# Performance work log

Measured on AMD Instinct MI355X. Metric: run time of the kernel, lower is better.

The kernel has to match this reference:

```python
import jax, jax.numpy as jnp
import numpy as np

_LN2 = 0.6931471805599453
B, N, C, R, K = 256, 4096, 256, 32, 128
MAX_SPAN = 20.0
W_WEIGHT, W_COACT, W_SPAN = 1.0, 1.0, 0.3


def setup_inputs() -> dict:
    key = jax.random.key(0)
    k1, k2, k3, k4, k5 = jax.random.split(key, 5)
    A = jax.random.normal(k1, (B, N), dtype=jnp.float32)            # accumulated atom activations
    span_t = jax.random.uniform(k2, (B,), dtype=jnp.float32) * MAX_SPAN
    proto_weights = jax.random.normal(k3, (C, N), dtype=jnp.float32) * 0.5
    proto_coact_U = jax.random.normal(k4, (C, N, R), dtype=jnp.float32) * 0.1
    proto_span = jax.random.normal(k5, (C,), dtype=jnp.float32) + 5.0
    return {"A": A, "span_t": span_t, "proto_weights": proto_weights,
            "proto_coact_U": proto_coact_U, "proto_span": proto_span}


def reference(A, span_t, proto_weights, proto_coact_U, proto_span):
    # CoActivationComputer._compute: top-K atoms per trajectory
    topk_vals, topk_idx = jax.lax.top_k(A, K)                       # [B,K], [B,K]

    # --- match_score ---
    proto_w = jax.nn.softplus(proto_weights) - _LN2                 # [C,N]
    score_w = A @ proto_w.T                                          # [B,C]
    score_w = score_w - jnp.mean(score_w, axis=1, keepdims=True)

    # CoActState.frob_inner_lowrank: gather U rows at top-k indices
    U_t = jnp.transpose(proto_coact_U, (1, 2, 0))                    # [N,R,C]
    U_topk = U_t[topk_idx]                                           # [B,K,R,C] (irregular gather)
    Au = jnp.einsum('bk,bkrc->brc', topk_vals, U_topk)               # [B,R,C]
    score_coact = jnp.sum(Au ** 2, axis=1) / (K * R + 1e-9)          # [B,C]

    span_norm = jnp.clip(span_t / MAX_SPAN, 0.0, 1.0)                # [B]
    proto_span_norm = jax.nn.sigmoid(proto_span)                     # [C]
    score_span = -jnp.abs(span_norm[:, None] - proto_span_norm[None, :])

    match_scores = W_WEIGHT * score_w + W_COACT * score_coact + W_SPAN * score_span  # [B,C]

    # --- compute_residual_score ---
    beta = jax.nn.softmax(match_scores, axis=-1)                     # [B,C]
    U_recon = jnp.einsum('bc,cnr->bnr', beta, proto_coact_U)         # [B,N,R]
    norm_Mhat = jnp.sum(topk_vals ** 2, axis=1)                      # [B]
    U_recon_topk = jnp.take_along_axis(U_recon, topk_idx[:, :, None], axis=1)  # [B,K,R]
    Au2 = jnp.einsum('bk,bkr->br', topk_vals, U_recon_topk)          # [B,R]
    cross = jnp.sum(Au2 ** 2, axis=1) / (K * R + 1e-9)
    norm_Mrecon = jnp.sum(U_recon ** 2, axis=(1, 2)) / (K * R + 1e-9)
    norm_Mhat_n = norm_Mhat / (K + 1e-9)
    residual = jnp.clip(norm_Mhat_n - 2.0 * cross + norm_Mrecon, 0.0, 10000.0)  # [B]
    return residual
```

## Files before the change

### kernel.cpp

```cpp
#include <hip/hip_runtime.h>
#include <math.h>

#define Bb 256
#define Nn 4096
#define Cc 256
#define Rr 32
#define Kk 128
#define Lflat (Nn * Rr)
#define LN2f 0.6931471805599453f
#define SKW 16

typedef unsigned short u16;
typedef __attribute__((ext_vector_type(8))) short short8b;
typedef __attribute__((ext_vector_type(4))) float f32x4;

typedef __attribute__((address_space(1))) const void* gas_t;
typedef __attribute__((address_space(3))) void* las_t;
__device__ __forceinline__ void gll16(const void* g, void* l) {
  __builtin_amdgcn_global_load_lds((gas_t)g, (las_t)l, 16, 0, 0);
}

__device__ inline u16 f2bf(float x) {
  unsigned u = __float_as_uint(x);
  unsigned r = (u + 0x7fffu + ((u >> 16) & 1u)) >> 16;
  return (u16)r;
}

__device__ inline unsigned f2u(float f) {
  unsigned b = __float_as_uint(f);
  return (b & 0x80000000u) ? ~b : (b | 0x80000000u);
}
__device__ inline float u2f(unsigned u) {
  unsigned b = (u & 0x80000000u) ? (u ^ 0x80000000u) : ~u;
  return __uint_as_float(b);
}

__global__ __launch_bounds__(256) void topk_kernel(const float* __restrict__ A,
                                                   u16* __restrict__ S,
                                                   float* __restrict__ mhat) {
  int b = blockIdx.x, t = threadIdx.x;
  int lane = t & 63, wave = t >> 6;
  const float* row = A + (size_t)b * Nn;
  u16* Srow = S + (size_t)b * Nn;
  short8b z = {0, 0, 0, 0, 0, 0, 0, 0};
  *(short8b*)(Srow + t * 16) = z;
  *(short8b*)(Srow + t * 16 + 8) = z;

  float f[16]; unsigned u[16];
#pragma unroll
  for (int j = 0; j < 4; ++j) {
    float4 v = ((const float4*)row)[j * 256 + t];
    f[j * 4 + 0] = v.x; f[j * 4 + 1] = v.y; f[j * 4 + 2] = v.z; f[j * 4 + 3] = v.w;
  }
#pragma unroll
  for (int j = 0; j < 16; ++j) u[j] = f2u(f[j]);

  __shared__ int hist[4][256];
  __shared__ int sufs[257];
  __shared__ int wtot[4];
  __shared__ int s_d, s_cg;
  __shared__ int s_eqidx[256];
  __shared__ int s_eqcnt;
  __shared__ float redQ[4];
  if (t == 0) s_eqcnt = 0;

  unsigned T = 0u;
  int cntG = 0;
#pragma unroll
  for (int p = 3; p >= 0; --p) {
    hist[0][t] = 0; hist[1][t] = 0; hist[2][t] = 0; hist[3][t] = 0;
    __syncthreads();
    unsigned mh = (p == 3) ? 0u : (0xFFFFFFFFu << (8 * (p + 1)));
    int* hw = hist[wave];
#pragma unroll
    for (int j = 0; j < 16; ++j)
      if (((u[j] ^ T) & mh) == 0) atomicAdd(&hw[(u[j] >> (8 * p)) & 255], 1);
    __syncthreads();
    int v = hist[0][t] + hist[1][t] + hist[2][t] + hist[3][t];
#pragma unroll
    for (int off = 1; off < 64; off <<= 1) {
      int tmp = __shfl_down(v, off, 64);
      if (lane + off < 64) v += tmp;
    }
    if (lane == 0) wtot[wave] = v;
    __syncthreads();
    for (int w2 = wave + 1; w2 < 4; ++w2) v += wtot[w2];
    sufs[t] = v;
    if (t == 0) sufs[256] = 0;
    __syncthreads();
    int nxt = sufs[t + 1];
    if ((cntG + v >= Kk) && (cntG + nxt < Kk)) { s_d = t; s_cg = cntG + nxt; }
    __syncthreads();
    T |= (unsigned)s_d << (8 * p);
    cntG = s_cg;
    __syncthreads();
  }
  float sq = 0.f;
#pragma unroll
  for (int j = 0; j < 16; ++j) {
    int idx = (j >> 2) * 1024 + t * 4 + (j & 3);
    if (u[j] > T) {
      Srow[idx] = f2bf(f[j]);
      sq += f[j] * f[j];
    } else if (u[j] == T) {
      int q2 = atomicAdd(&s_eqcnt, 1);
      if (q2 < 256) s_eqidx[q2] = idx;
    }
  }
#pragma unroll
  for (int off = 32; off; off >>= 1) sq += __shfl_xor(sq, off, 64);
  if (lane == 0) redQ[wave] = sq;
  __syncthreads();
  if (t == 0) {
    float tv = u2f(T);
    u16 tb = f2bf(tv);
    int need = Kk - cntG;
    int eq = min(s_eqcnt, 256);
    for (int s2 = 0; s2 < need; ++s2) {
      int best = 0x7fffffff, bi = 0;
      for (int jj = 0; jj < eq; ++jj)
        if (s_eqidx[jj] < best) { best = s_eqidx[jj]; bi = jj; }
      Srow[best] = tb;
      s_eqidx[bi] = 0x7fffffff;
    }
    mhat[b] = redQ[0] + redQ[1] + redQ[2] + redQ[3] + (float)need * tv * tv;
  }
}

__global__ __launch_bounds__(256) void u2t_kernel(const float* __restrict__ U,
                                                  u16* __restrict__ UT) {
  int c = blockIdx.x, nb = blockIdx.y, t = threadIdx.x;
  int r = t & 31, nblk = t >> 5;
  const float* Uc = U + (size_t)c * Lflat;
  u16* UTc = UT + (size_t)c * Lflat;
  for (int it = 0; it < 8; ++it) {
    int n0 = nb * 512 + it * 64 + nblk * 8;
    union { short8b v; u16 s[8]; } pk;
#pragma unroll
    for (int i = 0; i < 8; ++i)
      pk.s[i] = f2bf(Uc[(size_t)(n0 + i) * Rr + r]);
    *(short8b*)(UTc + (size_t)r * Nn + n0) = pk.v;
  }
}

__global__ __launch_bounds__(256) void scorew_mfma_kernel(const float* __restrict__ Ag,
                                                          const float* __restrict__ W,
                                                          float* __restrict__ SWp) {
  int ct = blockIdx.x, mt = blockIdx.y, ks = blockIdx.z;
  int t = threadIdx.x;
  int lane = t & 63, wave = t >> 6;
  int lo = lane & 15, hi = lane >> 4;
  int wr = wave >> 1, wc = wave & 1;
  __shared__ __align__(16) u16 As[64 * 64];
  __shared__ __align__(16) u16 Ws[64 * 64];
  f32x4 acc[2][2];
#pragma unroll
  for (int m = 0; m < 2; ++m)
#pragma unroll
    for (int n = 0; n < 2; ++n) acc[m][n] = (f32x4){0.f, 0.f, 0.f, 0.f};
  int kbase = ks * (Nn / SKW);
  for (int k0 = 0; k0 < Nn / SKW; k0 += 64) {
    for (int s = t; s < 1024; s += 256) {
      int panel = s >> 9;
      int sl = s & 511;
      int row = sl >> 3, q = sl & 7;
      union { short8b v; u16 u[8]; } pk;
      if (panel == 0) {
        const float* src = Ag + (size_t)(mt * 64 + row) * Nn + kbase + k0 + q * 8;
        float4 f0 = *(const float4*)src, f1 = *(const float4*)(src + 4);
        pk.u[0] = f2bf(f0.x); pk.u[1] = f2bf(f0.y); pk.u[2] = f2bf(f0.z); pk.u[3] = f2bf(f0.w);
        pk.u[4] = f2bf(f1.x); pk.u[5] = f2bf(f1.y); pk.u[6] = f2bf(f1.z); pk.u[7] = f2bf(f1.w);
        *(short8b*)(&As[row * 64 + ((q ^ (row & 7)) << 3)]) = pk.v;
      } else {
        const float* src = W + (size_t)(ct * 64 + row) * Nn + kbase + k0 + q * 8;
        float4 f0 = *(const float4*)src, f1 = *(const float4*)(src + 4);
        float w[8] = {f0.x, f0.y, f0.z, f0.w, f1.x, f1.y, f1.z, f1.w};
#pragma unroll
        for (int j = 0; j < 8; ++j)
          pk.u[j] = f2bf(fmaxf(w[j], 0.f) + log1pf(expf(-fabsf(w[j]))) - LN2f);
        *(short8b*)(&Ws[row * 64 + ((q ^ (row & 7)) << 3)]) = pk.v;
      }
    }
    __syncthreads();
#pragma unroll
    for (int kf = 0; kf < 2; ++kf) {
      int q = kf * 4 + hi;
      short8b af[2], bf[2];
#pragma unroll
      for (int m = 0; m < 2; ++m) {
        int row = wr * 32 + m * 16 + lo;
        af[m] = *(const short8b*)(&As[row * 64 + ((q ^ (row & 7)) << 3)]);
      }
#pragma unroll
      for (int n = 0; n < 2; ++n) {
        int row = wc * 32 + n * 16 + lo;
        bf[n] = *(const short8b*)(&Ws[row * 64 + ((q ^ (row & 7)) << 3)]);
      }
#pragma unroll
      for (int m = 0; m < 2; ++m)
#pragma unroll
        for (int n = 0; n < 2; ++n)
          acc[m][n] = __builtin_amdgcn_mfma_f32_16x16x32_bf16(af[m], bf[n], acc[m][n], 0, 0, 0);
    }
    __syncthreads();
  }
  float* o = SWp + (size_t)ks * (Bb * Cc);
#pragma unroll
  for (int m = 0; m < 2; ++m)
#pragma unroll
    for (int n = 0; n < 2; ++n)
#pragma unroll
      for (int r = 0; r < 4; ++r) {
        int b = mt * 64 + wr * 32 + m * 16 + hi * 4 + r;
        int c = ct * 64 + wc * 32 + n * 16 + lo;
        o[(size_t)b * Cc + c] = acc[m][n][r];
      }
}

__global__ __launch_bounds__(256) void gram_bf16_kernel(const u16* __restrict__ UT,
                                                        float* __restrict__ Gpart,
                                                        int kch) {
  int bx = blockIdx.x;
  int tile = bx % 3, chunk = bx / 3;
  int ti = (tile == 2) ? 1 : 0;
  int tj = (tile == 0) ? 0 : 1;
  bool diag = (tile != 1);
  int t = threadIdx.x, lane = t & 63, wave = t >> 6;
  int lo = lane & 15, hi = lane >> 4;
  int wr = wave >> 1, wc = wave & 1;
  __shared__ __align__(16) u16 lp[2][128 * 64];
  f32x4 acc[4][4];
#pragma unroll
  for (int m = 0; m < 4; ++m)
#pragma unroll
    for (int n = 0; n < 4; ++n) acc[m][n] = (f32x4){0.f, 0.f, 0.f, 0.f};
  int lrow = lane >> 3;
  int lchunk8 = ((lane & 7) ^ lrow) * 8;
  size_t kbase = (size_t)chunk * kch;
  for (int k0 = 0; k0 < kch; k0 += 64) {
    size_t kg = kbase + k0;
#pragma unroll
    for (int q = 0; q < 4; ++q) {
      int row = wave * 32 + q * 8;
      gll16(UT + (size_t)(ti * 128 + row + lrow) * Lflat + kg + lchunk8, &lp[0][row * 64]);
    }
    if (!diag) {
#pragma unroll
      for (int q = 0; q < 4; ++q) {
        int row = wave * 32 + q * 8;
        gll16(UT + (size_t)(tj * 128 + row + lrow) * Lflat + kg + lchunk8, &lp[1][row * 64]);
      }
    }
    __syncthreads();
#pragma unroll
    for (int ks = 0; ks < 2; ++ks) {
      short8b af[4], bfv[4];
#pragma unroll
      for (int m = 0; m < 4; ++m) {
        int row = wr * 64 + m * 16 + lo;
        af[m] = *(const short8b*)(&lp[0][row * 64 + (((ks * 4 + hi) ^ (row & 7)) << 3)]);
      }
      const u16* pb = diag ? lp[0] : lp[1];
#pragma unroll
      for (int n = 0; n < 4; ++n) {
        int row = wc * 64 + n * 16 + lo;
        bfv[n] = *(const short8b*)(&pb[row * 64 + (((ks * 4 + hi) ^ (row & 7)) << 3)]);
      }
#pragma unroll
      for (int m = 0; m < 4; ++m)
#pragma unroll
        for (int n = 0; n < 4; ++n)
          acc[m][n] = __builtin_amdgcn_mfma_f32_16x16x32_bf16(af[m], bfv[n], acc[m][n], 0, 0, 0);
    }
    __syncthreads();
  }
  float* gp = Gpart + (size_t)bx * 16384;
#pragma unroll
  for (int m = 0; m < 4; ++m)
#pragma unroll
    for (int n = 0; n < 4; ++n)
#pragma unroll
      for (int r = 0; r < 4; ++r) {
        int row = wr * 64 + m * 16 + hi * 4 + r;
        int col = wc * 64 + n * 16 + lo;
        gp[row * 128 + col] = acc[m][n][r];
      }
}

__global__ __launch_bounds__(256) void gram_mfma_kernel(const float* __restrict__ U,
                                                        float* __restrict__ Gpart,
                                                        int kch) {
  int bx = blockIdx.x;
  int tile = bx % 3;
  int chunk = bx / 3;
  int ti = (tile == 2) ? 1 : 0;
  int tj = (tile == 0) ? 0 : 1;
  bool diag = (tile != 1);
  int t = threadIdx.x;
  int lane = t & 63, wave = t >> 6;
  int lo = lane & 15, hi = lane >> 4;
  int wr = wave >> 1, wc = wave & 1;
  __shared__ __align__(16) u16 lp[2][128 * 64];
  size_t kbase = (size_t)chunk * kch;
  f32x4 acc[4][4];
#pragma unroll
  for (int m = 0; m < 4; ++m)
#pragma unroll
    for (int n = 0; n < 4; ++n) acc[m][n] = (f32x4){0.f, 0.f, 0.f, 0.f};
  int nslots = diag ? 1024 : 2048;
  for (int k0 = 0; k0 < kch; k0 += 64) {
    for (int s = t; s < nslots; s += 256) {
      int panel = s >> 10;
      int sl = s & 1023;
      int row = sl >> 3, q = sl & 7;
      int grow = (panel ? tj : ti) * 128 + row;
      const float* src = U + (size_t)grow * Lflat + kbase + k0 + q * 8;
      float4 f0 = *(const float4*)src;
      float4 f1 = *(const float4*)(src + 4);
      union { short8b v; u16 u[8]; } pk;
      pk.u[0] = f2bf(f0.x); pk.u[1] = f2bf(f0.y); pk.u[2] = f2bf(f0.z); pk.u[3] = f2bf(f0.w);
      pk.u[4] = f2bf(f1.x); pk.u[5] = f2bf(f1.y); pk.u[6] = f2bf(f1.z); pk.u[7] = f2bf(f1.w);
      *(short8b*)(&lp[panel][row * 64 + ((q ^ (row & 7)) << 3)]) = pk.v;
    }
    __syncthreads();
#pragma unroll
    for (int ks = 0; ks < 2; ++ks) {
      short8b af[4], bfv[4];
#pragma unroll
      for (int m = 0; m < 4; ++m) {
        int row = wr * 64 + m * 16 + lo;
        af[m] = *(const short8b*)(&lp[0][row * 64 + (((ks * 4 + hi) ^ (row & 7)) << 3)]);
      }
      const u16* pb = diag ? lp[0] : lp[1];
#pragma unroll
      for (int n = 0; n < 4; ++n) {
        int row = wc * 64 + n * 16 + lo;
        bfv[n] = *(const short8b*)(&pb[row * 64 + (((ks * 4 + hi) ^ (row & 7)) << 3)]);
      }
#pragma unroll
      for (int m = 0; m < 4; ++m)
#pragma unroll
        for (int n = 0; n < 4; ++n)
          acc[m][n] = __builtin_amdgcn_mfma_f32_16x16x32_bf16(af[m], bfv[n], acc[m][n], 0, 0, 0);
    }
    __syncthreads();
  }
  float* gp = Gpart + (size_t)bx * 16384;
#pragma unroll
  for (int m = 0; m < 4; ++m)
#pragma unroll
    for (int n = 0; n < 4; ++n)
#pragma unroll
      for (int r = 0; r < 4; ++r) {
        int row = wr * 64 + m * 16 + hi * 4 + r;
        int col = wc * 64 + n * 16 + lo;
        gp[row * 128 + col] = acc[m][n][r];
      }
}

__global__ __launch_bounds__(256) void gram_reduce_kernel(const float* __restrict__ Gpart,
                                                          float* __restrict__ G,
                                                          int nchunks) {
  int tile = blockIdx.x % 3, seg = blockIdx.x / 3;
  int ti = (tile == 2) ? 1 : 0;
  int tj = (tile == 0) ? 0 : 1;
  int e = seg * 1024 + threadIdx.x * 4;
  float4 s = {0.f, 0.f, 0.f, 0.f};
  for (int ch = 0; ch < nchunks; ++ch) {
    float4 v = *(const float4*)(Gpart + ((size_t)(ch * 3 + tile)) * 16384 + e);
    s.x += v.x; s.y += v.y; s.z += v.z; s.w += v.w;
  }
  int row = e >> 7, col = e & 127;
  int gi = ti * 128 + row, gj = tj * 128 + col;
  G[gi * Cc + gj + 0] = s.x;
  G[gi * Cc + gj + 1] = s.y;
  G[gi * Cc + gj + 2] = s.z;
  G[gi * Cc + gj + 3] = s.w;
  if (tile == 1) {
    G[(gj + 0) * Cc + gi] = s.x;
    G[(gj + 1) * Cc + gi] = s.y;
    G[(gj + 2) * Cc + gi] = s.z;
    G[(gj + 3) * Cc + gi] = s.w;
  }
}

__global__ __launch_bounds__(256) void au_gemm_kernel(const u16* __restrict__ S,
                                                      const u16* __restrict__ UT,
                                                      float* __restrict__ Au,
                                                      float* __restrict__ SC) {
  int jt = blockIdx.x, bt = blockIdx.y;
  int t = threadIdx.x, lane = t & 63, wave = t >> 6;
  int lo = lane & 15, hi = lane >> 4;
  int wr = wave >> 1, wc = wave & 1;
  __shared__ __align__(16) u16 Sa[128 * 64];
  __shared__ __align__(16) u16 Ub[64 * 64];
  f32x4 acc[4][2];
#pragma unroll
  for (int m = 0; m < 4; ++m)
#pragma unroll
    for (int n = 0; n < 2; ++n) acc[m][n] = (f32x4){0.f, 0.f, 0.f, 0.f};
  int lrow = lane >> 3;
  int lchunk8 = ((lane & 7) ^ lrow) * 8;
  for (int k0 = 0; k0 < Nn; k0 += 64) {
#pragma unroll
    for (int q = 0; q < 4; ++q) {
      int row = wave * 32 + q * 8;
      gll16(S + (size_t)(bt * 128 + row + lrow) * Nn + k0 + lchunk8, &Sa[row * 64]);
    }
#pragma unroll
    for (int q = 0; q < 2; ++q) {
      int row = wave * 16 + q * 8;
      gll16(UT + (size_t)(jt * 64 + row + lrow) * Nn + k0 + lchunk8, &Ub[row * 64]);
    }
    __syncthreads();
#pragma unroll
    for (int ks = 0; ks < 2; ++ks) {
      int q = ks * 4 + hi;
      short8b af[4], bfv[2];
#pragma unroll
      for (int m = 0; m < 4; ++m) {
        int r = wr * 64 + m * 16 + lo;
        af[m] = *(const short8b*)(&Sa[r * 64 + ((q ^ (r & 7)) << 3)]);
      }
#pragma unroll
      for (int n = 0; n < 2; ++n) {
        int r = wc * 32 + n * 16 + lo;
        bfv[n] = *(const short8b*)(&Ub[r * 64 + ((q ^ (r & 7)) << 3)]);
      }
#pragma unroll
      for (int m = 0; m < 4; ++m)
#pragma unroll
        for (int n = 0; n < 2; ++n)
          acc[m][n] = __builtin_amdgcn_mfma_f32_16x16x32_bf16(af[m], bfv[n], acc[m][n], 0, 0, 0);
    }
    __syncthreads();
  }
  int c = jt * 2 + wc;
#pragma unroll
  for (int m = 0; m < 4; ++m)
#pragma unroll
    for (int rr = 0; rr < 4; ++rr) {
      int b = bt * 128 + wr * 64 + m * 16 + hi * 4 + rr;
      float a0 = acc[m][0][rr], a1 = acc[m][1][rr];
      Au[((size_t)b * Cc + c) * Rr + lo]      = a0;
      Au[((size_t)b * Cc + c) * Rr + 16 + lo] = a1;
      float sq = a0 * a0 + a1 * a1;
      sq += __shfl_xor(sq, 1, 64);
      sq += __shfl_xor(sq, 2, 64);
      sq += __shfl_xor(sq, 4, 64);
      sq += __shfl_xor(sq, 8, 64);
      if (lo == 0) SC[(size_t)b * Cc + c] = sq * (1.f / (Kk * Rr));
    }
}

__global__ __launch_bounds__(256) void au_mfma_kernel(const float* __restrict__ U,
                                                      const u16* __restrict__ S,
                                                      float* __restrict__ Au,
                                                      float* __restrict__ SC) {
  int c = blockIdx.x, mb = blockIdx.y;
  int t = threadIdx.x;
  int lane = t & 63, wave = t >> 6;
  int lo = lane & 15, hi = lane >> 4;
  __shared__ __align__(16) u16 Ss[128 * 64];
  __shared__ __align__(16) u16 Us[32 * 64];
  f32x4 acc[2][2];
#pragma unroll
  for (int m = 0; m < 2; ++m)
#pragma unroll
    for (int n = 0; n < 2; ++n) acc[m][n] = (f32x4){0.f, 0.f, 0.f, 0.f};
  const float* Uc = U + (size_t)c * Lflat;
  for (int k0 = 0; k0 < Nn; k0 += 64) {
    for (int s = t; s < 1024; s += 256) {
      int row = s >> 3, q = s & 7;
      short8b v = *(const short8b*)(S + (size_t)(mb * 128 + row) * Nn + k0 + q * 8);
      *(short8b*)(&Ss[row * 64 + ((q ^ (row & 7)) << 3)]) = v;
    }
    for (int s = t; s < 512; s += 256) {
      int kk = s >> 3, rq = s & 7;
      float4 f = *(const float4*)(Uc + (size_t)(k0 + kk) * Rr + rq * 4);
      float fv[4] = {f.x, f.y, f.z, f.w};
#pragma unroll
      for (int j = 0; j < 4; ++j) {
        int r = rq * 4 + j;
        Us[r * 64 + (((kk >> 3) ^ (r & 7)) << 3) + (kk & 7)] = f2bf(fv[j]);
      }
    }
    __syncthreads();
#pragma unroll
    for (int kf = 0; kf < 2; ++kf) {
      int q = kf * 4 + hi;
      short8b af[2], bf[2];
#pragma unroll
      for (int m = 0; m < 2; ++m) {
        int row = wave * 32 + m * 16 + lo;
        af[m] = *(const short8b*)(&Ss[row * 64 + ((q ^ (row & 7)) << 3)]);
      }
#pragma unroll
      for (int n = 0; n < 2; ++n) {
        int row = n * 16 + lo;
        bf[n] = *(const short8b*)(&Us[row * 64 + ((q ^ (row & 7)) << 3)]);
      }
#pragma unroll
      for (int m = 0; m < 2; ++m)
#pragma unroll
        for (int n = 0; n < 2; ++n)
          acc[m][n] = __builtin_amdgcn_mfma_f32_16x16x32_bf16(af[m], bf[n], acc[m][n], 0, 0, 0);
    }
    __syncthreads();
  }
#pragma unroll
  for (int m = 0; m < 2; ++m) {
#pragma unroll
    for (int r = 0; r < 4; ++r) {
      int b = mb * 128 + wave * 32 + m * 16 + hi * 4 + r;
#pragma unroll
      for (int n = 0; n < 2; ++n) {
        int rr = n * 16 + lo;
        Au[((size_t)b * Cc + c) * Rr + rr] = acc[m][n][r];
      }
      float sq = acc[m][0][r] * acc[m][0][r] + acc[m][1][r] * acc[m][1][r];
      sq += __shfl_xor(sq, 1, 64);
      sq += __shfl_xor(sq, 2, 64);
      sq += __shfl_xor(sq, 4, 64);
      sq += __shfl_xor(sq, 8, 64);
      if (lo == 0) SC[(size_t)b * Cc + c] = sq * (1.f / (Kk * Rr));
    }
  }
}

__global__ __launch_bounds__(256) void softfin_kernel(const float* __restrict__ SWp,
                                                      const float* __restrict__ SC,
                                                      const float* __restrict__ span_t,
                                                      const float* __restrict__ PS,
                                                      const float* __restrict__ G,
                                                      const float* __restrict__ Au,
                                                      const float* __restrict__ mhat,
                                                      float* __restrict__ out) {
  int b = blockIdx.x, t = threadIdx.x;
  int lane = t & 63, wave = t >> 6;
  __shared__ float redM[4], redS[4], redA[4];
  __shared__ float sb[Cc];
  __shared__ float au2[8][32];
  float span_norm = fminf(fmaxf(span_t[b] * (1.f / 20.f), 0.f), 1.f);
  float psn = 1.f / (1.f + expf(-PS[t]));
  float m = 0.f;
#pragma unroll
  for (int kc = 0; kc < SKW; ++kc) m += SWp[(size_t)kc * (Bb * Cc) + b * Cc + t];
  m += SC[b * Cc + t] - 0.3f * fabsf(span_norm - psn);
  float mx = m;
#pragma unroll
  for (int off = 32; off; off >>= 1) mx = fmaxf(mx, __shfl_xor(mx, off, 64));
  if (lane == 0) redM[wave] = mx;
  __syncthreads();
  mx = fmaxf(fmaxf(redM[0], redM[1]), fmaxf(redM[2], redM[3]));
  float e = expf(m - mx);
  float s = e;
#pragma unroll
  for (int off = 32; off; off >>= 1) s += __shfl_xor(s, off, 64);
  if (lane == 0) redS[wave] = s;
  __syncthreads();
  s = redS[0] + redS[1] + redS[2] + redS[3];
  float beta_t = e / s;
  sb[t] = beta_t;
  __syncthreads();
  float w = 0.f;
#pragma unroll 8
  for (int c = 0; c < Cc; ++c) w = fmaf(sb[c], G[c * Cc + t], w);
  float pr = beta_t * w;
  int r = t & 31, g = t >> 5;
  float pp = 0.f;
#pragma unroll 8
  for (int cc = 0; cc < 32; ++cc) {
    int c = cc * 8 + g;
    pp = fmaf(sb[c], Au[((size_t)b * Cc + c) * Rr + r], pp);
  }
  au2[g][r] = pp;
  float x = pr;
#pragma unroll
  for (int off = 32; off; off >>= 1) x += __shfl_xor(x, off, 64);
  if (lane == 0) redA[wave] = x;
  __syncthreads();
  float recon = (redA[0] + redA[1] + redA[2] + redA[3]) * (1.f / 4096.f);
  float cr = 0.f;
  if (t < 32) {
    float a2 = au2[0][t] + au2[1][t] + au2[2][t] + au2[3][t]
             + au2[4][t] + au2[5][t] + au2[6][t] + au2[7][t];
    cr = a2 * a2;
  }
#pragma unroll
  for (int off = 16; off; off >>= 1) cr += __shfl_xor(cr, off, 64);
  if (t == 0) {
    cr *= (1.f / 4096.f);
    float res = mhat[b] * (1.f / 128.f) - 2.f * cr + recon;
    out[b] = fminf(fmaxf(res, 0.f), 10000.f);
  }
}

extern "C" void kernel_launch(void* const* d_in, const int* in_sizes, int n_in,
                              void* d_out, int out_size, void* d_ws, size_t ws_size,
                              hipStream_t stream) {
  const float* A      = (const float*)d_in[0];
  const float* span_t = (const float*)d_in[1];
  const float* W      = (const float*)d_in[2];
  const float* U      = (const float*)d_in[3];
  const float* PS     = (const float*)d_in[4];
  float* out = (float*)d_out;

  char* p = (char*)d_ws;
  float* mhat = (float*)p; p += (size_t)Bb * 4;
  float* SWp  = (float*)p; p += (size_t)SKW * Bb * Cc * 4;
  float* SC   = (float*)p; p += (size_t)Bb * Cc * 4;
  float* G    = (float*)p; p += (size_t)Cc * Cc * 4;
  u16*   S    = (u16*)p;   p += (size_t)Bb * Nn * 2;
  float* Au   = (float*)p; p += (size_t)Bb * Cc * Rr * 4;
  size_t fixed = (size_t)(p - (char*)d_ws);
  size_t UTsz = (size_t)Cc * Lflat * 2;
  bool planA = ws_size >= fixed + UTsz + (size_t)3 * 8 * 16384 * 4;

  topk_kernel<<<dim3(Bb), dim3(256), 0, stream>>>(A, S, mhat);
  scorew_mfma_kernel<<<dim3(4, 4, SKW), dim3(256), 0, stream>>>(A, W, SWp);

  if (planA) {
    u16* UT = (u16*)p; p += UTsz;
    size_t used = fixed + UTsz;
    int nchunks = 64;
    while (nchunks > 8 && used + (size_t)(3 * nchunks) * 16384 * 4 > ws_size) nchunks >>= 1;
    float* Gpart = (float*)p;
    u2t_kernel<<<dim3(Cc, 8), dim3(256), 0, stream>>>(U, UT);
    gram_bf16_kernel<<<dim3(3 * nchunks), dim3(256), 0, stream>>>(UT, Gpart, Lflat / nchunks);
    gram_reduce_kernel<<<dim3(48), dim3(256), 0, stream>>>(Gpart, G, nchunks);
    au_gemm_kernel<<<dim3(128, 2), dim3(256), 0, stream>>>(S, UT, Au, SC);
  } else {
    int nchunks = 64;
    while (nchunks > 8 && fixed + (size_t)(3 * nchunks) * 16384 * 4 > ws_size) nchunks >>= 1;
    float* Gpart = (float*)p;
    gram_mfma_kernel<<<dim3(3 * nchunks), dim3(256), 0, stream>>>(U, Gpart, Lflat / nchunks);
    gram_reduce_kernel<<<dim3(48), dim3(256), 0, stream>>>(Gpart, G, nchunks);
    au_mfma_kernel<<<dim3(Cc, 2), dim3(256), 0, stream>>>(U, S, Au, SC);
  }

  softfin_kernel<<<dim3(Bb), dim3(256), 0, stream>>>(SWp, SC, span_t, PS, G, Au, mhat, out);
}
```

Before: 193.3 us.

## Drop bf16 transposed copy of U; read fp32 U directly in gram and Au kernels

Removes the u2t pre-pass that converted U into a transposed bf16 buffer, along with the bf16 gram and Au GEMM kernels that consumed it. The gram is now always computed from fp32 U with more chunks (128). A new Au kernel loads per-prototype fp32 U columns, converts them to bf16 in registers and stores them into swizzled LDS, while S is staged with direct global-to-LDS loads. The goal is to skip writing and re-reading a 16MB intermediate, at the cost of extra conversion work and strided fp32 reads inside the GEMM kernels.

```diff
diff --git a/kernel.cpp b/kernel.cpp
--- a/kernel.cpp
+++ b/kernel.cpp
@@ -124,22 +124,6 @@
       s_eqidx[bi] = 0x7fffffff;
     }
     mhat[b] = redQ[0] + redQ[1] + redQ[2] + redQ[3] + (float)need * tv * tv;
-  }
-}
-
-__global__ __launch_bounds__(256) void u2t_kernel(const float* __restrict__ U,
-                                                  u16* __restrict__ UT) {
-  int c = blockIdx.x, nb = blockIdx.y, t = threadIdx.x;
-  int r = t & 31, nblk = t >> 5;
-  const float* Uc = U + (size_t)c * Lflat;
-  u16* UTc = UT + (size_t)c * Lflat;
-  for (int it = 0; it < 8; ++it) {
-    int n0 = nb * 512 + it * 64 + nblk * 8;
-    union { short8b v; u16 s[8]; } pk;
-#pragma unroll
-    for (int i = 0; i < 8; ++i)
-      pk.s[i] = f2bf(Uc[(size_t)(n0 + i) * Rr + r]);
-    *(short8b*)(UTc + (size_t)r * Nn + n0) = pk.v;
   }
 }
 
@@ -217,76 +201,6 @@
       }
 }
 
-__global__ __launch_bounds__(256) void gram_bf16_kernel(const u16* __restrict__ UT,
-                                                        float* __restrict__ Gpart,
-                                                        int kch) {
-  int bx = blockIdx.x;
-  int tile = bx % 3, chunk = bx / 3;
-  int ti = (tile == 2) ? 1 : 0;
-  int tj = (tile == 0) ? 0 : 1;
-  bool diag = (tile != 1);
-  int t = threadIdx.x, lane = t & 63, wave = t >> 6;
-  int lo = lane & 15, hi = lane >> 4;
-  int wr = wave >> 1, wc = wave & 1;
-  __shared__ __align__(16) u16 lp[2][128 * 64];
-  f32x4 acc[4][4];
-#pragma unroll
-  for (int m = 0; m < 4; ++m)
-#pragma unroll
-    for (int n = 0; n < 4; ++n) acc[m][n] = (f32x4){0.f, 0.f, 0.f, 0.f};
-  int lrow = lane >> 3;
-  int lchunk8 = ((lane & 7) ^ lrow) * 8;
-  size_t kbase = (size_t)chunk * kch;
-  for (int k0 = 0; k0 < kch; k0 += 64) {
-    size_t kg = kbase + k0;
-#pragma unroll
-    for (int q = 0; q < 4; ++q) {
-      int row = wave * 32 + q * 8;
-      gll16(UT + (size_t)(ti * 128 + row + lrow) * Lflat + kg + lchunk8, &lp[0][row * 64]);
-    }
-    if (!diag) {
-#pragma unroll
-      for (int q = 0; q < 4; ++q) {
-        int row = wave * 32 + q * 8;
-        gll16(UT + (size_t)(tj * 128 + row + lrow) * Lflat + kg + lchunk8, &lp[1][row * 64]);
-      }
-    }
-    __syncthreads();
-#pragma unroll
-    for (int ks = 0; ks < 2; ++ks) {
-      short8b af[4], bfv[4];
-#pragma unroll
-      for (int m = 0; m < 4; ++m) {
-        int row = wr * 64 + m * 16 + lo;
-        af[m] = *(const short8b*)(&lp[0][row * 64 + (((ks * 4 + hi) ^ (row & 7)) << 3)]);
-      }
-      const u16* pb = diag ? lp[0] : lp[1];
-#pragma unroll
-      for (int n = 0; n < 4; ++n) {
-        int row = wc * 64 + n * 16 + lo;
-        bfv[n] = *(const short8b*)(&pb[row * 64 + (((ks * 4 + hi) ^ (row & 7)) << 3)]);
-      }
-#pragma unroll
-      for (int m = 0; m < 4; ++m)
-#pragma unroll
-        for (int n = 0; n < 4; ++n)
-          acc[m][n] = __builtin_amdgcn_mfma_f32_16x16x32_bf16(af[m], bfv[n], acc[m][n], 0, 0, 0);
-    }
-    __syncthreads();
-  }
-  float* gp = Gpart + (size_t)bx * 16384;
-#pragma unroll
-  for (int m = 0; m < 4; ++m)
-#pragma unroll
-    for (int n = 0; n < 4; ++n)
-#pragma unroll
-      for (int r = 0; r < 4; ++r) {
-        int row = wr * 64 + m * 16 + hi * 4 + r;
-        int col = wc * 64 + n * 16 + lo;
-        gp[row * 128 + col] = acc[m][n][r];
-      }
-}
-
 __global__ __launch_bounds__(256) void gram_mfma_kernel(const float* __restrict__ U,
                                                         float* __restrict__ Gpart,
                                                         int kch) {
@@ -384,141 +298,78 @@
   }
 }
 
-__global__ __launch_bounds__(256) void au_gemm_kernel(const u16* __restrict__ S,
-                                                      const u16* __restrict__ UT,
+__global__ __launch_bounds__(256) void au_fp32_kernel(const float* __restrict__ U,
+                                                      const u16* __restrict__ S,
                                                       float* __restrict__ Au,
                                                       float* __restrict__ SC) {
-  int jt = blockIdx.x, bt = blockIdx.y;
+  int c = blockIdx.x, bt = blockIdx.y;
   int t = threadIdx.x, lane = t & 63, wave = t >> 6;
   int lo = lane & 15, hi = lane >> 4;
-  int wr = wave >> 1, wc = wave & 1;
   __shared__ __align__(16) u16 Sa[128 * 64];
-  __shared__ __align__(16) u16 Ub[64 * 64];
-  f32x4 acc[4][2];
-#pragma unroll
-  for (int m = 0; m < 4; ++m)
+  __shared__ __align__(16) u16 Ub[32 * 64];
+  f32x4 acc[2][2];
+#pragma unroll
+  for (int m = 0; m < 2; ++m)
 #pragma unroll
     for (int n = 0; n < 2; ++n) acc[m][n] = (f32x4){0.f, 0.f, 0.f, 0.f};
+
   int lrow = lane >> 3;
-  int lchunk8 = ((lane & 7) ^ lrow) * 8;
+  int lchunk = (lane & 7) ^ lrow;
+  const u16* sbase[4];
+#pragma unroll
+  for (int q = 0; q < 4; ++q) {
+    int row = wave * 32 + q * 8;
+    sbase[q] = S + (size_t)(bt * 128 + row + lrow) * Nn + lchunk * 8;
+  }
+  int ur = t & 31, uq = t >> 5;
+  const float* ucol = U + (size_t)c * Lflat + ur;
+  int uswz = (uq ^ (ur & 7)) << 3;
+
   for (int k0 = 0; k0 < Nn; k0 += 64) {
 #pragma unroll
     for (int q = 0; q < 4; ++q) {
       int row = wave * 32 + q * 8;
-      gll16(S + (size_t)(bt * 128 + row + lrow) * Nn + k0 + lchunk8, &Sa[row * 64]);
-    }
-#pragma unroll
-    for (int q = 0; q < 2; ++q) {
-      int row = wave * 16 + q * 8;
-      gll16(UT + (size_t)(jt * 64 + row + lrow) * Nn + k0 + lchunk8, &Ub[row * 64]);
+      gll16(sbase[q] + k0, &Sa[row * 64]);
+    }
+    {
+      union { short8b v; u16 s[8]; } pk;
+#pragma unroll
+      for (int i = 0; i < 8; ++i)
+        pk.s[i] = f2bf(ucol[(size_t)(k0 + uq * 8 + i) * 32]);
+      *(short8b*)(&Ub[ur * 64 + uswz]) = pk.v;
     }
     __syncthreads();
 #pragma unroll
     for (int ks = 0; ks < 2; ++ks) {
       int q = ks * 4 + hi;
-      short8b af[4], bfv[2];
-#pragma unroll
-      for (int m = 0; m < 4; ++m) {
-        int r = wr * 64 + m * 16 + lo;
-        af[m] = *(const short8b*)(&Sa[r * 64 + ((q ^ (r & 7)) << 3)]);
+      short8b af[2], bf[2];
+#pragma unroll
+      for (int m = 0; m < 2; ++m) {
+        int row = wave * 32 + m * 16 + lo;
+        af[m] = *(const short8b*)(&Sa[row * 64 + ((q ^ (row & 7)) << 3)]);
       }
 #pragma unroll
       for (int n = 0; n < 2; ++n) {
-        int r = wc * 32 + n * 16 + lo;
-        bfv[n] = *(const short8b*)(&Ub[r * 64 + ((q ^ (r & 7)) << 3)]);
-      }
-#pragma unroll
-      for (int m = 0; m < 4; ++m)
+        int rr = n * 16 + lo;
+        bf[n] = *(const short8b*)(&Ub[rr * 64 + ((q ^ (rr & 7)) << 3)]);
+      }
+#pragma unroll
+      for (int m = 0; m < 2; ++m)
 #pragma unroll
         for (int n = 0; n < 2; ++n)
-          acc[m][n] = __builtin_amdgcn_mfma_f32_16x16x32_bf16(af[m], bfv[n], acc[m][n], 0, 0, 0);
-    }
-    __syncthreads();
-  }
-  int c = jt * 2 + wc;
-#pragma unroll
-  for (int m = 0; m < 4; ++m)
-#pragma unroll
-    for (int rr = 0; rr < 4; ++rr) {
-      int b = bt * 128 + wr * 64 + m * 16 + hi * 4 + rr;
-      float a0 = acc[m][0][rr], a1 = acc[m][1][rr];
+          acc[m][n] = __builtin_amdgcn_mfma_f32_16x16x32_bf16(af[m], bf[n], acc[m][n], 0, 0, 0);
+    }
+    __syncthreads();
+  }
+#pragma unroll
+  for (int m = 0; m < 2; ++m) {
+#pragma unroll
+    for (int r = 0; r < 4; ++r) {
+      int b = bt * 128 + wave * 32 + m * 16 + hi * 4 + r;
+      float a0 = acc[m][0][r], a1 = acc[m][1][r];
       Au[((size_t)b * Cc + c) * Rr + lo]      = a0;
       Au[((size_t)b * Cc + c) * Rr + 16 + lo] = a1;
       float sq = a0 * a0 + a1 * a1;
-      sq += __shfl_xor(sq, 1, 64);
-      sq += __shfl_xor(sq, 2, 64);
-      sq += __shfl_xor(sq, 4, 64);
-      sq += __shfl_xor(sq, 8, 64);
-      if (lo == 0) SC[(size_t)b * Cc + c] = sq * (1.f / (Kk * Rr));
-    }
-}
-
-__global__ __launch_bounds__(256) void au_mfma_kernel(const float* __restrict__ U,
-                                                      const u16* __restrict__ S,
-                                                      float* __restrict__ Au,
-                                                      float* __restrict__ SC) {
-  int c = blockIdx.x, mb = blockIdx.y;
-  int t = threadIdx.x;
-  int lane = t & 63, wave = t >> 6;
-  int lo = lane & 15, hi = lane >> 4;
-  __shared__ __align__(16) u16 Ss[128 * 64];
-  __shared__ __align__(16) u16 Us[32 * 64];
-  f32x4 acc[2][2];
-#pragma unroll
-  for (int m = 0; m < 2; ++m)
-#pragma unroll
-    for (int n = 0; n < 2; ++n) acc[m][n] = (f32x4){0.f, 0.f, 0.f, 0.f};
-  const float* Uc = U + (size_t)c * Lflat;
-  for (int k0 = 0; k0 < Nn; k0 += 64) {
-    for (int s = t; s < 1024; s += 256) {
-      int row = s >> 3, q = s & 7;
-      short8b v = *(const short8b*)(S + (size_t)(mb * 128 + row) * Nn + k0 + q * 8);
-      *(short8b*)(&Ss[row * 64 + ((q ^ (row & 7)) << 3)]) = v;
-    }
-    for (int s = t; s < 512; s += 256) {
-      int kk = s >> 3, rq = s & 7;
-      float4 f = *(const float4*)(Uc + (size_t)(k0 + kk) * Rr + rq * 4);
-      float fv[4] = {f.x, f.y, f.z, f.w};
-#pragma unroll
-      for (int j = 0; j < 4; ++j) {
-        int r = rq * 4 + j;
-        Us[r * 64 + (((kk >> 3) ^ (r & 7)) << 3) + (kk & 7)] = f2bf(fv[j]);
-      }
-    }
-    __syncthreads();
-#pragma unroll
-    for (int kf = 0; kf < 2; ++kf) {
-      int q = kf * 4 + hi;
-      short8b af[2], bf[2];
-#pragma unroll
-      for (int m = 0; m < 2; ++m) {
-        int row = wave * 32 + m * 16 + lo;
-        af[m] = *(const short8b*)(&Ss[row * 64 + ((q ^ (row & 7)) << 3)]);
-      }
-#pragma unroll
-      for (int n = 0; n < 2; ++n) {
-        int row = n * 16 + lo;
-        bf[n] = *(const short8b*)(&Us[row * 64 + ((q ^ (row & 7)) << 3)]);
-      }
-#pragma unroll
-      for (int m = 0; m < 2; ++m)
-#pragma unroll
-        for (int n = 0; n < 2; ++n)
-          acc[m][n] = __builtin_amdgcn_mfma_f32_16x16x32_bf16(af[m], bf[n], acc[m][n], 0, 0, 0);
-    }
-    __syncthreads();
-  }
-#pragma unroll
-  for (int m = 0; m < 2; ++m) {
-#pragma unroll
-    for (int r = 0; r < 4; ++r) {
-      int b = mb * 128 + wave * 32 + m * 16 + hi * 4 + r;
-#pragma unroll
-      for (int n = 0; n < 2; ++n) {
-        int rr = n * 16 + lo;
-        Au[((size_t)b * Cc + c) * Rr + rr] = acc[m][n][r];
-      }
-      float sq = acc[m][0][r] * acc[m][0][r] + acc[m][1][r] * acc[m][1][r];
       sq += __shfl_xor(sq, 1, 64);
       sq += __shfl_xor(sq, 2, 64);
       sq += __shfl_xor(sq, 4, 64);
@@ -614,30 +465,14 @@
   u16*   S    = (u16*)p;   p += (size_t)Bb * Nn * 2;
   float* Au   = (float*)p; p += (size_t)Bb * Cc * Rr * 4;
   size_t fixed = (size_t)(p - (char*)d_ws);
-  size_t UTsz = (size_t)Cc * Lflat * 2;
-  bool planA = ws_size >= fixed + UTsz + (size_t)3 * 8 * 16384 * 4;
+  int nchunks = 128;
+  while (nchunks > 8 && fixed + (size_t)(3 * nchunks) * 16384 * 4 > ws_size) nchunks >>= 1;
+  float* Gpart = (float*)p;
 
   topk_kernel<<<dim3(Bb), dim3(256), 0, stream>>>(A, S, mhat);
   scorew_mfma_kernel<<<dim3(4, 4, SKW), dim3(256), 0, stream>>>(A, W, SWp);
-
-  if (planA) {
-    u16* UT = (u16*)p; p += UTsz;
-    size_t used = fixed + UTsz;
-    int nchunks = 64;
-    while (nchunks > 8 && used + (size_t)(3 * nchunks) * 16384 * 4 > ws_size) nchunks >>= 1;
-    float* Gpart = (float*)p;
-    u2t_kernel<<<dim3(Cc, 8), dim3(256), 0, stream>>>(U, UT);
-    gram_bf16_kernel<<<dim3(3 * nchunks), dim3(256), 0, stream>>>(UT, Gpart, Lflat / nchunks);
-    gram_reduce_kernel<<<dim3(48), dim3(256), 0, stream>>>(Gpart, G, nchunks);
-    au_gemm_kernel<<<dim3(128, 2), dim3(256), 0, stream>>>(S, UT, Au, SC);
-  } else {
-    int nchunks = 64;
-    while (nchunks > 8 && fixed + (size_t)(3 * nchunks) * 16384 * 4 > ws_size) nchunks >>= 1;
-    float* Gpart = (float*)p;
-    gram_mfma_kernel<<<dim3(3 * nchunks), dim3(256), 0, stream>>>(U, Gpart, Lflat / nchunks);
-    gram_reduce_kernel<<<dim3(48), dim3(256), 0, stream>>>(Gpart, G, nchunks);
-    au_mfma_kernel<<<dim3(Cc, 2), dim3(256), 0, stream>>>(U, S, Au, SC);
-  }
-
+  gram_mfma_kernel<<<dim3(3 * nchunks), dim3(256), 0, stream>>>(U, Gpart, Lflat / nchunks);
+  au_fp32_kernel<<<dim3(Cc, 2), dim3(256), 0, stream>>>(U, S, Au, SC);
+  gram_reduce_kernel<<<dim3(48), dim3(256), 0, stream>>>(Gpart, G, nchunks);
   softfin_kernel<<<dim3(Bb), dim3(256), 0, stream>>>(SWp, SC, span_t, PS, G, Au, mhat, out);
 }
```

Result: slower. 217.2 us (+12.4%).
